# Performance work log

Hardware: AMD Instinct MI355X
Metric: run time of the kernel (lower is better)

Reference implementation:

```python
import jax, jax.numpy as jnp
import numpy as np
from jax.lax import associative_scan

D_H = 1024

def _binary_operator(e_i, e_j):
    a_i, kv_i = e_i
    a_j, kv_j = e_j
    return (a_j * a_i, a_j * kv_i + kv_j)

def setup_inputs() -> dict:
    key = jax.random.key(0)
    k1, k2 = jax.random.split(key)
    x = jax.random.normal(k1, (4, 4096, 3 * D_H), dtype=jnp.float32)
    carry = jax.random.normal(k2, (4, D_H), dtype=jnp.float32)
    return {"x": x, "carry": carry}

def reference(x, carry):
    d_h = D_H
    inp = jnp.tanh(x[:, :, :d_h])                      # (B, S, d_h)
    gates = jax.nn.sigmoid(x[:, :, d_h:])              # (B, S, 2*d_h)
    input_gate, output_gate = jnp.split(gates, 2, axis=-1)
    forget_gate = 1.0 - input_gate                     # tied gates
    scan_ins = inp * input_gate                        # (B, S, d_h)
    # inject carry at t=0: h_0 = f_0*carry + i_0*in_0
    scan_ins = scan_ins.at[:, 0, :].set(scan_ins[:, 0, :] + carry * forget_gate[:, 0, :])
    _, h = associative_scan(_binary_operator, (forget_gate, scan_ins), axis=1)
    y = jnp.tanh(h) * output_gate                      # (B, S, d_h)
    h_last = h[:, -1, :]
    return (h_last, y)
```

## Files before the change

### kernel.cpp

```cpp
#include <hip/hip_runtime.h>


#define B_SZ 4
#define T_LEN 4096
#define DH 1024
#define ROW4 (3 * DH / 4)
#define CHUNKS 128
#define CLEN (T_LEN / CHUNKS)

__device__ __forceinline__ float fsig(float v) {
    return __builtin_amdgcn_rcpf(1.0f + __expf(-v));
}
__device__ __forceinline__ float ftanh(float v) {
    return 1.0f - 2.0f * __builtin_amdgcn_rcpf(__expf(2.0f * v) + 1.0f);
}

__global__ __launch_bounds__(256) void glru_pass1(const float* __restrict__ x,
                                                  float4* __restrict__ Aag,
                                                  float4* __restrict__ Bag) {
    const int c = blockIdx.x;
    const int b = blockIdx.y;
    const int d4 = threadIdx.x;
    const float4* base = (const float4*)x + (size_t)(b * T_LEN + c * CLEN) * ROW4;

    float4 A = make_float4(1.f, 1.f, 1.f, 1.f);
    float4 Bv = make_float4(0.f, 0.f, 0.f, 0.f);
    for (int t = 0; t < CLEN; ++t) {
        const float4 vi = base[(size_t)t * ROW4 + d4];
        const float4 vg = base[(size_t)t * ROW4 + 256 + d4];
        {
            float ig = fsig(vg.x); float a = 1.f - ig;
            A.x *= a; Bv.x = a * Bv.x + ftanh(vi.x) * ig;
        }
        {
            float ig = fsig(vg.y); float a = 1.f - ig;
            A.y *= a; Bv.y = a * Bv.y + ftanh(vi.y) * ig;
        }
        {
            float ig = fsig(vg.z); float a = 1.f - ig;
            A.z *= a; Bv.z = a * Bv.z + ftanh(vi.z) * ig;
        }
        {
            float ig = fsig(vg.w); float a = 1.f - ig;
            A.w *= a; Bv.w = a * Bv.w + ftanh(vi.w) * ig;
        }
    }
    const int o = (b * CHUNKS + c) * 256 + d4;
    Aag[o] = A;
    Bag[o] = Bv;
}

__global__ __launch_bounds__(256) void glru_pass2(const float* __restrict__ Aag,
                                                  const float* __restrict__ Bag,
                                                  const float* __restrict__ carry,
                                                  float* __restrict__ hinit,
                                                  float* __restrict__ hlast) {
    const int idx = blockIdx.x * 256 + threadIdx.x;
    const int b = idx >> 10;
    const int d = idx & 1023;
    float h = carry[idx];
    #pragma unroll 8
    for (int c = 0; c < CHUNKS; ++c) {
        const int o = (b * CHUNKS + c) * 1024 + d;
        hinit[o] = h;
        h = Aag[o] * h + Bag[o];
    }
    hlast[idx] = h;
}

__global__ __launch_bounds__(256) void glru_pass3(const float* __restrict__ x,
                                                  const float4* __restrict__ hinit,
                                                  float4* __restrict__ y) {
    const int c = blockIdx.x;
    const int b = blockIdx.y;
    const int d4 = threadIdx.x;
    const float4* base = (const float4*)x + (size_t)(b * T_LEN + c * CLEN) * ROW4;
    float4* yb = y + (size_t)(b * T_LEN + c * CLEN) * 256;

    float4 h = hinit[(b * CHUNKS + c) * 256 + d4];
    for (int t = 0; t < CLEN; ++t) {
        const float4 vi = base[(size_t)t * ROW4 + d4];
        const float4 vg = base[(size_t)t * ROW4 + 256 + d4];
        const float4 vo = base[(size_t)t * ROW4 + 512 + d4];
        float4 out;
        {
            float ig = fsig(vg.x); float a = 1.f - ig;
            h.x = a * h.x + ftanh(vi.x) * ig;
            out.x = ftanh(h.x) * fsig(vo.x);
        }
        {
            float ig = fsig(vg.y); float a = 1.f - ig;
            h.y = a * h.y + ftanh(vi.y) * ig;
            out.y = ftanh(h.y) * fsig(vo.y);
        }
        {
            float ig = fsig(vg.z); float a = 1.f - ig;
            h.z = a * h.z + ftanh(vi.z) * ig;
            out.z = ftanh(h.z) * fsig(vo.z);
        }
        {
            float ig = fsig(vg.w); float a = 1.f - ig;
            h.w = a * h.w + ftanh(vi.w) * ig;
            out.w = ftanh(h.w) * fsig(vo.w);
        }
        yb[(size_t)t * 256 + d4] = out;
    }
}

extern "C" void kernel_launch(void* const* d_in, const int* in_sizes, int n_in,
                              void* d_out, int out_size, void* d_ws, size_t ws_size,
                              hipStream_t stream) {
    const float* x = (const float*)d_in[0];
    const float* carry = (const float*)d_in[1];

    float* hlast = (float*)d_out;
    float4* y = (float4*)((float*)d_out + B_SZ * DH);

    float* Aag = (float*)d_ws;
    float* Bag = Aag + (size_t)B_SZ * CHUNKS * DH;
    float* hinit = Bag + (size_t)B_SZ * CHUNKS * DH;

    glru_pass1<<<dim3(CHUNKS, B_SZ), 256, 0, stream>>>(x, (float4*)Aag, (float4*)Bag);
    glru_pass2<<<16, 256, 0, stream>>>(Aag, Bag, carry, hinit, hlast);
    glru_pass3<<<dim3(CHUNKS, B_SZ), 256, 0, stream>>>(x, (const float4*)hinit, y);
}
```

Measured before the change: 316.8 us.

## Use finer chunks with hierarchical two-level carry scan and preloaded inputs

Raises the chunk count from 128 to 512 so passes 1 and 3 launch more blocks and have shorter serial loops. The serial middle scan, which previously ran in only 16 blocks, becomes three kernels: a parallel reduce into super-chunks, a short serial scan over the super-chunks, and a parallel fan-out that writes each chunk's initial state. Passes 1 and 3 also load all of a chunk's timesteps into registers before computing, and pass 3 writes y with nontemporal stores. The cost is two extra kernel launches and more workspace traffic for the chunk aggregates.

```diff
diff --git a/kernel.cpp b/kernel.cpp
--- a/kernel.cpp
+++ b/kernel.cpp
@@ -5,14 +5,25 @@
 #define T_LEN 4096
 #define DH 1024
 #define ROW4 (3 * DH / 4)
-#define CHUNKS 128
+#define CHUNKS 512
 #define CLEN (T_LEN / CHUNKS)
+#define SUBC 8
+#define SUPERS (CHUNKS / SUBC)
+
+typedef float vf4 __attribute__((ext_vector_type(4)));
 
 __device__ __forceinline__ float fsig(float v) {
     return __builtin_amdgcn_rcpf(1.0f + __expf(-v));
 }
 __device__ __forceinline__ float ftanh(float v) {
     return 1.0f - 2.0f * __builtin_amdgcn_rcpf(__expf(2.0f * v) + 1.0f);
+}
+
+__device__ __forceinline__ void step_ab(float xi, float xg, float& A, float& Bv) {
+    const float ig = fsig(xg);
+    const float a = 1.f - ig;
+    A *= a;
+    Bv = a * Bv + ftanh(xi) * ig;
 }
 
 __global__ __launch_bounds__(256) void glru_pass1(const float* __restrict__ x,
@@ -23,49 +34,83 @@
     const int d4 = threadIdx.x;
     const float4* base = (const float4*)x + (size_t)(b * T_LEN + c * CLEN) * ROW4;
 
+    float4 vi[CLEN], vg[CLEN];
+    #pragma unroll
+    for (int t = 0; t < CLEN; ++t) {
+        vi[t] = base[(size_t)t * ROW4 + d4];
+        vg[t] = base[(size_t)t * ROW4 + 256 + d4];
+    }
+
     float4 A = make_float4(1.f, 1.f, 1.f, 1.f);
     float4 Bv = make_float4(0.f, 0.f, 0.f, 0.f);
+    #pragma unroll
     for (int t = 0; t < CLEN; ++t) {
-        const float4 vi = base[(size_t)t * ROW4 + d4];
-        const float4 vg = base[(size_t)t * ROW4 + 256 + d4];
-        {
-            float ig = fsig(vg.x); float a = 1.f - ig;
-            A.x *= a; Bv.x = a * Bv.x + ftanh(vi.x) * ig;
-        }
-        {
-            float ig = fsig(vg.y); float a = 1.f - ig;
-            A.y *= a; Bv.y = a * Bv.y + ftanh(vi.y) * ig;
-        }
-        {
-            float ig = fsig(vg.z); float a = 1.f - ig;
-            A.z *= a; Bv.z = a * Bv.z + ftanh(vi.z) * ig;
-        }
-        {
-            float ig = fsig(vg.w); float a = 1.f - ig;
-            A.w *= a; Bv.w = a * Bv.w + ftanh(vi.w) * ig;
-        }
+        step_ab(vi[t].x, vg[t].x, A.x, Bv.x);
+        step_ab(vi[t].y, vg[t].y, A.y, Bv.y);
+        step_ab(vi[t].z, vg[t].z, A.z, Bv.z);
+        step_ab(vi[t].w, vg[t].w, A.w, Bv.w);
     }
     const int o = (b * CHUNKS + c) * 256 + d4;
     Aag[o] = A;
     Bag[o] = Bv;
 }
 
-__global__ __launch_bounds__(256) void glru_pass2(const float* __restrict__ Aag,
-                                                  const float* __restrict__ Bag,
-                                                  const float* __restrict__ carry,
-                                                  float* __restrict__ hinit,
-                                                  float* __restrict__ hlast) {
+__global__ __launch_bounds__(256) void glru_p2a(const float* __restrict__ Aag,
+                                                const float* __restrict__ Bag,
+                                                float* __restrict__ Asup,
+                                                float* __restrict__ Bsup) {
+    const int tid = blockIdx.x * 256 + threadIdx.x;
+    const int d = tid & (DH - 1);
+    const int su = (tid >> 10) & (SUPERS - 1);
+    const int b = tid >> 16;
+
+    float As = 1.f, Bs = 0.f;
+    #pragma unroll
+    for (int j = 0; j < SUBC; ++j) {
+        const size_t o = ((size_t)(b * CHUNKS + su * SUBC + j) << 10) + d;
+        const float a = Aag[o];
+        As *= a;
+        Bs = a * Bs + Bag[o];
+    }
+    const int so = (b * SUPERS + su) * DH + d;
+    Asup[so] = As;
+    Bsup[so] = Bs;
+}
+
+__global__ __launch_bounds__(256) void glru_p2b(const float* __restrict__ Asup,
+                                                const float* __restrict__ Bsup,
+                                                const float* __restrict__ carry,
+                                                float* __restrict__ hsup,
+                                                float* __restrict__ hlast) {
     const int idx = blockIdx.x * 256 + threadIdx.x;
     const int b = idx >> 10;
-    const int d = idx & 1023;
+    const int d = idx & (DH - 1);
     float h = carry[idx];
     #pragma unroll 8
-    for (int c = 0; c < CHUNKS; ++c) {
-        const int o = (b * CHUNKS + c) * 1024 + d;
+    for (int s = 0; s < SUPERS; ++s) {
+        const int o = (b * SUPERS + s) * DH + d;
+        hsup[o] = h;
+        h = Asup[o] * h + Bsup[o];
+    }
+    hlast[idx] = h;
+}
+
+__global__ __launch_bounds__(256) void glru_p2c(const float* __restrict__ Aag,
+                                                const float* __restrict__ Bag,
+                                                const float* __restrict__ hsup,
+                                                float* __restrict__ hinit) {
+    const int tid = blockIdx.x * 256 + threadIdx.x;
+    const int d = tid & (DH - 1);
+    const int su = (tid >> 10) & (SUPERS - 1);
+    const int b = tid >> 16;
+
+    float h = hsup[(b * SUPERS + su) * DH + d];
+    #pragma unroll
+    for (int j = 0; j < SUBC; ++j) {
+        const size_t o = ((size_t)(b * CHUNKS + su * SUBC + j) << 10) + d;
         hinit[o] = h;
         h = Aag[o] * h + Bag[o];
     }
-    hlast[idx] = h;
 }
 
 __global__ __launch_bounds__(256) void glru_pass3(const float* __restrict__ x,
@@ -77,33 +122,41 @@
     const float4* base = (const float4*)x + (size_t)(b * T_LEN + c * CLEN) * ROW4;
     float4* yb = y + (size_t)(b * T_LEN + c * CLEN) * 256;
 
+    float4 vi[CLEN], vg[CLEN];
+    #pragma unroll
+    for (int t = 0; t < CLEN; ++t) {
+        vi[t] = base[(size_t)t * ROW4 + d4];
+        vg[t] = base[(size_t)t * ROW4 + 256 + d4];
+    }
     float4 h = hinit[(b * CHUNKS + c) * 256 + d4];
+
+    #pragma unroll
     for (int t = 0; t < CLEN; ++t) {
-        const float4 vi = base[(size_t)t * ROW4 + d4];
-        const float4 vg = base[(size_t)t * ROW4 + 256 + d4];
         const float4 vo = base[(size_t)t * ROW4 + 512 + d4];
         float4 out;
         {
-            float ig = fsig(vg.x); float a = 1.f - ig;
-            h.x = a * h.x + ftanh(vi.x) * ig;
+            float ig = fsig(vg[t].x); float a = 1.f - ig;
+            h.x = a * h.x + ftanh(vi[t].x) * ig;
             out.x = ftanh(h.x) * fsig(vo.x);
         }
         {
-            float ig = fsig(vg.y); float a = 1.f - ig;
-            h.y = a * h.y + ftanh(vi.y) * ig;
+            float ig = fsig(vg[t].y); float a = 1.f - ig;
+            h.y = a * h.y + ftanh(vi[t].y) * ig;
             out.y = ftanh(h.y) * fsig(vo.y);
         }
         {
-            float ig = fsig(vg.z); float a = 1.f - ig;
-            h.z = a * h.z + ftanh(vi.z) * ig;
+            float ig = fsig(vg[t].z); float a = 1.f - ig;
+            h.z = a * h.z + ftanh(vi[t].z) * ig;
             out.z = ftanh(h.z) * fsig(vo.z);
         }
         {
-            float ig = fsig(vg.w); float a = 1.f - ig;
-            h.w = a * h.w + ftanh(vi.w) * ig;
+            float ig = fsig(vg[t].w); float a = 1.f - ig;
+            h.w = a * h.w + ftanh(vi[t].w) * ig;
             out.w = ftanh(h.w) * fsig(vo.w);
         }
-        yb[(size_t)t * 256 + d4] = out;
+        vf4 outv;
+        outv.x = out.x; outv.y = out.y; outv.z = out.z; outv.w = out.w;
+        __builtin_nontemporal_store(outv, (vf4*)&yb[(size_t)t * 256 + d4]);
     }
 }
 
@@ -119,8 +172,13 @@
     float* Aag = (float*)d_ws;
     float* Bag = Aag + (size_t)B_SZ * CHUNKS * DH;
     float* hinit = Bag + (size_t)B_SZ * CHUNKS * DH;
+    float* Asup = hinit + (size_t)B_SZ * CHUNKS * DH;
+    float* Bsup = Asup + (size_t)B_SZ * SUPERS * DH;
+    float* hsup = Bsup + (size_t)B_SZ * SUPERS * DH;
 
     glru_pass1<<<dim3(CHUNKS, B_SZ), 256, 0, stream>>>(x, (float4*)Aag, (float4*)Bag);
-    glru_pass2<<<16, 256, 0, stream>>>(Aag, Bag, carry, hinit, hlast);
+    glru_p2a<<<(B_SZ * SUPERS * DH) / 256, 256, 0, stream>>>(Aag, Bag, Asup, Bsup);
+    glru_p2b<<<16, 256, 0, stream>>>(Asup, Bsup, carry, hsup, hlast);
+    glru_p2c<<<(B_SZ * SUPERS * DH) / 256, 256, 0, stream>>>(Aag, Bag, hsup, hinit);
     glru_pass3<<<dim3(CHUNKS, B_SZ), 256, 0, stream>>>(x, (const float4*)hinit, y);
 }
```

Result: no change. 318.0 us (+0.4%).
